# Performance work log

Hardware: AMD Instinct MI355X
Metric: run time of the kernel (lower is better)

## Reference

```python
import jax, jax.numpy as jnp
import numpy as np

NUM_HEADS = 8
LN_EPS = 1e-5


def _positional_encoding(pos_index, d_pe):
    # standard sinusoidal PE, positions start at 1; sin on even cols, cos on odd cols
    pos = pos_index.astype(jnp.float32)[:, None]                      # [N,1]
    freqs = jnp.exp(jnp.arange(0, d_pe, 2, dtype=jnp.float32) * (-np.log(10000.0) / d_pe))
    ang = pos * freqs                                                 # [N, d_pe//2]
    return jnp.stack([jnp.sin(ang), jnp.cos(ang)], axis=-1).reshape(pos.shape[0], d_pe)


def setup_inputs() -> dict:
    EMB, POS, DEV, B = 512, 64, 448, 64
    lengths = np.where(np.arange(B) % 2 == 0, 128, 256)               # ragged group sizes
    state_index = jnp.asarray(np.concatenate([[0], np.cumsum(lengths)]), dtype=jnp.int32)
    total = int(lengths.sum())                                        # 12288
    ks = jax.random.split(jax.random.key(0), 5)
    in_dim = DEV + POS
    return {
        "states": jax.random.normal(ks[0], (total, DEV), jnp.float32),
        "state_index": state_index,
        "W1": jax.random.normal(ks[1], (EMB, in_dim), jnp.float32) / np.sqrt(in_dim),
        "b1": jnp.zeros((EMB,), jnp.float32),
        "in_w": jax.random.normal(ks[2], (3 * EMB, EMB), jnp.float32) / np.sqrt(EMB),
        "in_b": jnp.zeros((3 * EMB,), jnp.float32),
        "out_w": jax.random.normal(ks[3], (EMB, EMB), jnp.float32) / np.sqrt(EMB),
        "out_b": jnp.zeros((EMB,), jnp.float32),
        "gamma": jnp.ones((EMB,), jnp.float32),
        "beta": jnp.zeros((EMB,), jnp.float32),
    }


def reference(states, state_index, W1, b1, in_w, in_b, out_w, out_b, gamma, beta):
    # --- static ragged bookkeeping from the int offsets (host-side) ---
    si = np.asarray(state_index)
    lengths = si[1:] - si[:-1]
    b = len(lengths)
    max_d = int(lengths.max())
    batch_index = jnp.asarray(np.repeat(np.arange(b), lengths), jnp.int32)   # [N]
    pos_np = np.concatenate([np.arange(1, l + 1) for l in lengths])
    pos_index = jnp.asarray(pos_np, jnp.int32)                               # [N], 1-based
    seq_idx = pos_index - 1                                                  # [N], 0-based slot

    E = W1.shape[0]
    d_pe = W1.shape[1] - states.shape[1]
    hd = E // NUM_HEADS

    # embedding MLP
    pe = _positional_encoding(pos_index, d_pe)
    x = jnp.concatenate([states, pe], axis=1)                                # [N, dev+pe]
    emb = jax.nn.leaky_relu(x @ W1.T + b1, 0.01)                             # [N, E]

    # scatter ragged tokens into padded [b, max_d, E] (zero filler, as in _reshape)
    dense = jnp.zeros((b, max_d, E), emb.dtype).at[batch_index, seq_idx].set(emb)

    # MultiheadAttention (batch_first, no padding mask -- faithful to original)
    qkv = dense @ in_w.T + in_b                                              # [b, md, 3E]
    q, k, v = jnp.split(qkv, 3, axis=-1)
    q = q.reshape(b, max_d, NUM_HEADS, hd)
    k = k.reshape(b, max_d, NUM_HEADS, hd)
    v = v.reshape(b, max_d, NUM_HEADS, hd)
    scores = jnp.einsum("bqhd,bkhd->bhqk", q, k) / np.sqrt(hd)
    attn = jax.nn.softmax(scores, axis=-1)
    ctx = jnp.einsum("bhqk,bkhd->bqhd", attn, v).reshape(b, max_d, E)
    mha_out = ctx @ out_w.T + out_b

    # residual + LayerNorm
    res = mha_out + dense
    mu = res.mean(axis=-1, keepdims=True)
    var = ((res - mu) ** 2).mean(axis=-1, keepdims=True)
    norm = (res - mu) / jnp.sqrt(var + LN_EPS) * gamma + beta

    # gather valid rows back out and concat with pre-attention embeddings
    sel = norm[batch_index, seq_idx]                                         # [N, E]
    return jnp.concatenate([emb, sel], axis=1)                               # [N, 2E]
```

## Files before the change

kernel.cpp:

```cpp
#include <hip/hip_runtime.h>

typedef unsigned short u16;
typedef __attribute__((ext_vector_type(8))) short bf16x8;
typedef __attribute__((ext_vector_type(4))) float f32x4;

__device__ __forceinline__ float bf2f(u16 u) {
    union { unsigned int i; float f; } v; v.i = ((unsigned int)u) << 16; return v.f;
}
__device__ __forceinline__ u16 f2bf(float f) {
    union { float f; unsigned int i; } v; v.f = f;
    unsigned int x = v.i;
    return (u16)((x + 0x7FFFu + ((x >> 16) & 1u)) >> 16);
}
__device__ __forceinline__ unsigned int f2bf_pk(float a, float b) {
    unsigned int r;
    asm("v_cvt_pk_bf16_f32 %0, %1, %2" : "=v"(r) : "v"(a), "v"(b));
    return r;
}

__device__ __forceinline__ bool probe_f32(const void* gamma) {
    return *(const unsigned int*)gamma == 0x3F800000u;
}
__device__ __forceinline__ float load1(const void* p, int i, bool f32) {
    return f32 ? ((const float*)p)[i] : bf2f(((const u16*)p)[i]);
}
__device__ __forceinline__ uint4 load8(const void* p, size_t e, bool f32) {
    if (f32) {
        const float* q = (const float*)p + e;
        float4 a = *(const float4*)q;
        float4 b = *(const float4*)(q + 4);
        uint4 r; u16* rp = (u16*)&r;
        rp[0] = f2bf(a.x); rp[1] = f2bf(a.y); rp[2] = f2bf(a.z); rp[3] = f2bf(a.w);
        rp[4] = f2bf(b.x); rp[5] = f2bf(b.y); rp[6] = f2bf(b.z); rp[7] = f2bf(b.w);
        return r;
    }
    return *(const uint4*)((const u16*)p + e);
}

__device__ __forceinline__ void glds16(const u16* g, u16* l) {
    __builtin_amdgcn_global_load_lds(
        (const __attribute__((address_space(1))) void*)g,
        (__attribute__((address_space(3))) void*)l, 16, 0, 0);
}

#define NTOK   12288
#define BATCH  64
#define MAXD   256
#define EMB    512
#define DEV    448

__global__ __launch_bounds__(64) void prep_xin(
        const void* __restrict__ states, const int* __restrict__ si,
        const void* __restrict__ W1, const void* __restrict__ in_w,
        const void* __restrict__ out_w, const void* __restrict__ b1,
        const void* __restrict__ in_b, const void* __restrict__ out_b,
        const void* __restrict__ gamma, const void* __restrict__ beta,
        u16* __restrict__ W1b, u16* __restrict__ in_wb, u16* __restrict__ out_wb,
        float* __restrict__ b1f, float* __restrict__ in_bf, float* __restrict__ out_bf,
        float* __restrict__ gf, float* __restrict__ bfv, u16* __restrict__ xin)
{
    bool f32 = probe_f32(gamma);
    int t = threadIdx.x;
    if (blockIdx.x < 2567) {
        int r = blockIdx.x;
        if (r < 512) {
            *(uint4*)&W1b[(size_t)r * 512 + t * 8] = load8(W1, (size_t)r * 512 + t * 8, f32);
        } else if (r < 2048) {
            int rc = r - 512;
            int h = rc / 192, rr = rc - h * 192;
            int part = rr >> 6, d = rc & 63;
            int orig = part * 512 + h * 64 + d;
            *(uint4*)&in_wb[(size_t)rc * 512 + t * 8] = load8(in_w, (size_t)orig * 512 + t * 8, f32);
        } else if (r < 2560) {
            int rc = r - 2048;
            *(uint4*)&out_wb[(size_t)rc * 512 + t * 8] = load8(out_w, (size_t)rc * 512 + t * 8, f32);
        } else if (r == 2560) {
            #pragma unroll
            for (int u = 0; u < 8; ++u) b1f[t * 8 + u] = load1(b1, t * 8 + u, f32);
        } else if (r < 2564) {
            int base = (r - 2561) * 512 + t * 8;
            #pragma unroll
            for (int u = 0; u < 8; ++u) {
                int j = base + u;
                int h = j / 192, rr = j - h * 192;
                int part = rr >> 6, d = j & 63;
                int orig = part * 512 + h * 64 + d;
                in_bf[j] = load1(in_b, orig, f32);
            }
        } else if (r == 2564) {
            #pragma unroll
            for (int u = 0; u < 8; ++u) out_bf[t * 8 + u] = load1(out_b, t * 8 + u, f32);
        } else if (r == 2565) {
            #pragma unroll
            for (int u = 0; u < 8; ++u) gf[t * 8 + u] = load1(gamma, t * 8 + u, f32);
        } else {
            #pragma unroll
            for (int u = 0; u < 8; ++u) bfv[t * 8 + u] = load1(beta, t * 8 + u, f32);
        }
    } else {
        int n = blockIdx.x - 2567;
        __shared__ int ssi[65];
        ssi[t] = si[t];
        if (t == 0) ssi[64] = si[64];
        __syncthreads();
        int lo = 0, hi = 64;
        while (hi - lo > 1) { int mid = (lo + hi) >> 1; if (ssi[mid] <= n) lo = mid; else hi = mid; }
        float pos = (float)(n - ssi[lo] + 1);
        if (t < 56) {
            *(uint4*)&xin[(size_t)n * 512 + t * 8] = load8(states, (size_t)n * DEV + t * 8, f32);
        } else {
            int j0 = (t - 56) * 8;
            uint4 vu; u16* vp = (u16*)&vu;
            #pragma unroll
            for (int jj = 0; jj < 8; ++jj) {
                int j = j0 + jj;
                int i = j >> 1;
                float freq = __expf(-0.2878231366f * (float)i);
                float ang = pos * freq;
                vp[jj] = f2bf((j & 1) ? cosf(ang) : sinf(ang));
            }
            *(uint4*)&xin[(size_t)n * 512 + DEV + j0] = vu;
        }
    }
}

template<int MODE>
__global__ __launch_bounds__(256) void gemm_glds(
        const u16* __restrict__ A, const u16* __restrict__ B,
        const float* __restrict__ bias, u16* __restrict__ C)
{
    constexpr int LDC = (MODE == 1) ? 1536 : 512;
    __shared__ __align__(16) u16 Ash[128 * 32];
    __shared__ __align__(16) u16 Bsh[128 * 32];
    __shared__ __align__(16) u16 Csh[4 * 32 * 72];

    int tid = threadIdx.x;
    int bm0 = blockIdx.y * 128, bn0 = blockIdx.x * 128;
    int lane = tid & 63, w = tid >> 6;
    int wm = (w >> 1) * 64, wn = (w & 1) * 64;
    int q = lane >> 4, m16 = lane & 15;
    int lr = lane >> 2, lc = (lane & 3) * 8;

    f32x4 acc[4][4];
    #pragma unroll
    for (int i = 0; i < 4; ++i)
        #pragma unroll
        for (int j = 0; j < 4; ++j) acc[i][j] = (f32x4){0.f, 0.f, 0.f, 0.f};

    const u16* Ab = A + (size_t)(bm0 + w * 16 + lr) * 512 + lc;
    const u16* Bb = B + (size_t)(bn0 + w * 16 + lr) * 512 + lc;
    u16* AshW = &Ash[(w * 16) * 32];
    u16* BshW = &Bsh[(w * 16) * 32];

    for (int k0 = 0; k0 < 512; k0 += 32) {
        __syncthreads();
        glds16(Ab + k0, AshW);
        glds16(Ab + (size_t)64 * 512 + k0, AshW + 64 * 32);
        glds16(Bb + k0, BshW);
        glds16(Bb + (size_t)64 * 512 + k0, BshW + 64 * 32);
        __syncthreads();
        bf16x8 af[4], bfr[4];
        #pragma unroll
        for (int i = 0; i < 4; ++i)
            af[i] = *(const bf16x8*)&Ash[(wm + i * 16 + m16) * 32 + q * 8];
        #pragma unroll
        for (int j = 0; j < 4; ++j)
            bfr[j] = *(const bf16x8*)&Bsh[(wn + j * 16 + m16) * 32 + q * 8];
        #pragma unroll
        for (int i = 0; i < 4; ++i)
            #pragma unroll
            for (int j = 0; j < 4; ++j)
                acc[i][j] = __builtin_amdgcn_mfma_f32_16x16x32_bf16(af[i], bfr[j], acc[i][j], 0, 0, 0);
    }

    u16* cw = &Csh[w * 32 * 72];
    float bv[4];
    #pragma unroll
    for (int j = 0; j < 4; ++j) bv[j] = bias[bn0 + wn + j * 16 + m16];

    int rrl = lane >> 3;
    int rcc = (lane & 7) * 8;

    #pragma unroll
    for (int ch = 0; ch < 2; ++ch) {
        #pragma unroll
        for (int ii = 0; ii < 2; ++ii) {
            int i = ch * 2 + ii;
            #pragma unroll
            for (int j = 0; j < 4; ++j) {
                float v0 = acc[i][j][0] + bv[j];
                float v1 = acc[i][j][1] + bv[j];
                float v2 = acc[i][j][2] + bv[j];
                float v3 = acc[i][j][3] + bv[j];
                if constexpr (MODE == 0) {
                    v0 = v0 >= 0.f ? v0 : 0.01f * v0;
                    v1 = v1 >= 0.f ? v1 : 0.01f * v1;
                    v2 = v2 >= 0.f ? v2 : 0.01f * v2;
                    v3 = v3 >= 0.f ? v3 : 0.01f * v3;
                }
                unsigned int pk01 = f2bf_pk(v0, v1);
                unsigned int pk23 = f2bf_pk(v2, v3);
                int rb = ii * 16 + q * 4;
                int cl = j * 16 + m16;
                cw[(rb + 0) * 72 + cl] = (u16)pk01;
                cw[(rb + 1) * 72 + cl] = (u16)(pk01 >> 16);
                cw[(rb + 2) * 72 + cl] = (u16)pk23;
                cw[(rb + 3) * 72 + cl] = (u16)(pk23 >> 16);
            }
        }
        #pragma unroll
        for (int p = 0; p < 4; ++p) {
            int row_l = p * 8 + rrl;
            uint4 v = *(const uint4*)&cw[row_l * 72 + rcc];
            int grow = bm0 + wm + ch * 32 + row_l;
            *(uint4*)&C[(size_t)grow * LDC + bn0 + wn + rcc] = v;
        }
    }
}

template<int LEN>
__global__ __launch_bounds__(512) void attn_mfma(
        const u16* __restrict__ qkv, const int* __restrict__ si,
        const float* __restrict__ in_bf, u16* __restrict__ ctx)
{
    constexpr int NT   = LEN / 16;
    constexpr int KS   = LEN / 32;
    constexpr int NPAD = 256 - LEN;
    constexpr int KSTR = 72;
    constexpr int VTS  = LEN + 8;

    __shared__ __align__(16) u16 Ksh[LEN * KSTR];
    __shared__ __align__(16) u16 Vt[64 * VTS];
    __shared__ __align__(16) u16 PshBuf[8 * 16 * VTS];
    __shared__ float kbsh[64];
    __shared__ float apsh[8][16];

    int h = blockIdx.x;
    int b = blockIdx.y * 2 + (LEN == 256 ? 1 : 0);
    int tid = threadIdx.x;
    int tok0 = si[b];
    int bb = h * 192;

    if (NPAD > 0 && tid < 64) kbsh[tid] = in_bf[bb + 64 + tid];

    constexpr int nIter = LEN * 8 / 512;
    #pragma unroll
    for (int it = 0; it < nIter; ++it) {
        int idx = tid + it * 512;
        int row = idx >> 3, c8 = (idx & 7) * 8;
        const u16* src = qkv + (size_t)(tok0 + row) * 1536 + bb;
        uint4 kv = *(const uint4*)(src + 64 + c8);
        *(uint4*)&Ksh[row * KSTR + c8] = kv;
        uint4 vv = *(const uint4*)(src + 128 + c8);
        const unsigned int* vw = (const unsigned int*)&vv;
        #pragma unroll
        for (int u = 0; u < 4; ++u)
            *(unsigned int*)&PshBuf[row * 66 + c8 + 2 * u] = vw[u];
    }
    __syncthreads();
    constexpr int SHIFT = (LEN == 256) ? 7 : 6;
    constexpr int tIter = (64 * (LEN / 2)) / 512;
    #pragma unroll
    for (int it = 0; it < tIter; ++it) {
        int idx = tid + it * 512;
        int d = idx >> SHIFT, kp = idx & (LEN / 2 - 1);
        unsigned int lo = PshBuf[(2 * kp) * 66 + d];
        unsigned int hi = PshBuf[(2 * kp + 1) * 66 + d];
        *(unsigned int*)&Vt[d * VTS + 2 * kp] = (hi << 16) | lo;
    }
    __syncthreads();

    int lane = tid & 63, w = tid >> 6;
    int m16 = lane & 15, quad = lane >> 4;
    int wq = w >> 2, wr = w & 3;
    int qt = (LEN == 256) ? blockIdx.z * 2 + wq : wq;
    u16* Psh = &PshBuf[w * 16 * VTS];

    int qrow = qt * 64 + wr * 16 + m16;
    const u16* qptr = qkv + (size_t)(tok0 + qrow) * 1536 + bb;
    bf16x8 aq0 = *(const bf16x8*)(qptr + quad * 8);
    bf16x8 aq1 = *(const bf16x8*)(qptr + 32 + quad * 8);

    if (NPAD > 0) {
        float apv = 0.f;
        #pragma unroll
        for (int j = 0; j < 8; ++j) {
            apv += bf2f((u16)aq0[j]) * kbsh[quad * 8 + j];
            apv += bf2f((u16)aq1[j]) * kbsh[32 + quad * 8 + j];
        }
        apv += __shfl_xor(apv, 16);
        apv += __shfl_xor(apv, 32);
        if (lane < 16) apsh[w][lane] = apv * 0.125f;
    }

    f32x4 sfr[NT];
    #pragma unroll
    for (int nt = 0; nt < NT; ++nt) sfr[nt] = (f32x4){0.f, 0.f, 0.f, 0.f};
    #pragma unroll
    for (int nt = 0; nt < NT; ++nt) {
        const u16* kr = &Ksh[(nt * 16 + m16) * KSTR + quad * 8];
        bf16x8 bk0 = *(const bf16x8*)(kr);
        bf16x8 bk1 = *(const bf16x8*)(kr + 32);
        sfr[nt] = __builtin_amdgcn_mfma_f32_16x16x32_bf16(aq0, bk0, sfr[nt], 0, 0, 0);
        sfr[nt] = __builtin_amdgcn_mfma_f32_16x16x32_bf16(aq1, bk1, sfr[nt], 0, 0, 0);
    }

    float pwv[4];
    #pragma unroll
    for (int reg = 0; reg < 4; ++reg) {
        float mx = -3.0e38f;
        #pragma unroll
        for (int nt = 0; nt < NT; ++nt) mx = fmaxf(mx, sfr[nt][reg]);
        mx *= 0.125f;
        float ap = 0.f;
        if (NPAD > 0) { ap = apsh[w][quad * 4 + reg]; mx = fmaxf(mx, ap); }
        #pragma unroll
        for (int off = 8; off >= 1; off >>= 1) mx = fmaxf(mx, __shfl_xor(mx, off));
        float p[NT];
        float sum = 0.f;
        #pragma unroll
        for (int nt = 0; nt < NT; ++nt) {
            p[nt] = __expf(sfr[nt][reg] * 0.125f - mx);
            sum += p[nt];
        }
        #pragma unroll
        for (int off = 8; off >= 1; off >>= 1) sum += __shfl_xor(sum, off);
        float padw = (NPAD > 0) ? (float)NPAD * __expf(ap - mx) : 0.f;
        float inv = __frcp_rn(sum + padw);
        pwv[reg] = padw * inv;
        #pragma unroll
        for (int nt = 0; nt < NT; ++nt)
            Psh[(quad * 4 + reg) * VTS + nt * 16 + m16] = f2bf(p[nt] * inv);
    }

    f32x4 ob[4];
    #pragma unroll
    for (int nt = 0; nt < 4; ++nt) ob[nt] = (f32x4){0.f, 0.f, 0.f, 0.f};
    #pragma unroll
    for (int ks = 0; ks < KS; ++ks) {
        bf16x8 af = *(const bf16x8*)&Psh[m16 * VTS + ks * 32 + quad * 8];
        #pragma unroll
        for (int nt = 0; nt < 4; ++nt) {
            bf16x8 bv = *(const bf16x8*)&Vt[(nt * 16 + m16) * VTS + ks * 32 + quad * 8];
            ob[nt] = __builtin_amdgcn_mfma_f32_16x16x32_bf16(af, bv, ob[nt], 0, 0, 0);
        }
    }

    int orow = tok0 + qt * 64 + wr * 16;
    #pragma unroll
    for (int nt = 0; nt < 4; ++nt) {
        int d = nt * 16 + m16;
        float vbv = (NPAD > 0) ? in_bf[bb + 128 + d] : 0.f;
        #pragma unroll
        for (int reg = 0; reg < 4; ++reg) {
            float val = ob[nt][reg];
            if (NPAD > 0) val += pwv[reg] * vbv;
            ctx[(size_t)(orow + quad * 4 + reg) * 512 + h * 64 + d] = f2bf(val);
        }
    }
}

__global__ __launch_bounds__(64) void ln_out(
        const u16* __restrict__ mha, const u16* __restrict__ emb,
        const float* __restrict__ gf, const float* __restrict__ bfv,
        void* __restrict__ out, const void* __restrict__ gamma)
{
    int n = blockIdx.x, lane = threadIdx.x;
    bool f32 = probe_f32(gamma);
    size_t base = (size_t)n * EMB + lane * 8;
    uint4 ev = *(const uint4*)&emb[base];
    uint4 mv = *(const uint4*)&mha[base];
    const u16* ep = (const u16*)&ev;
    const u16* mp = (const u16*)&mv;
    float e[8], r[8];
    float sum = 0.f, sq = 0.f;
    #pragma unroll
    for (int u = 0; u < 8; ++u) {
        e[u] = bf2f(ep[u]);
        r[u] = bf2f(mp[u]) + e[u];
        sum += r[u];
        sq += r[u] * r[u];
    }
    #pragma unroll
    for (int off = 32; off >= 1; off >>= 1) {
        sum += __shfl_xor(sum, off);
        sq  += __shfl_xor(sq, off);
    }
    float mu = sum * (1.f / 512.f);
    float var = sq * (1.f / 512.f) - mu * mu;
    float rstd = rsqrtf(var + 1e-5f);

    float4 g0 = *(const float4*)(gf + lane * 8);
    float4 g1 = *(const float4*)(gf + lane * 8 + 4);
    float4 be0 = *(const float4*)(bfv + lane * 8);
    float4 be1 = *(const float4*)(bfv + lane * 8 + 4);
    float g[8] = {g0.x, g0.y, g0.z, g0.w, g1.x, g1.y, g1.z, g1.w};
    float bb[8] = {be0.x, be0.y, be0.z, be0.w, be1.x, be1.y, be1.z, be1.w};
    float o[8];
    #pragma unroll
    for (int u = 0; u < 8; ++u) o[u] = (r[u] - mu) * rstd * g[u] + bb[u];

    if (f32) {
        float* op = (float*)out + (size_t)n * 1024 + lane * 8;
        *(float4*)(op)           = make_float4(e[0], e[1], e[2], e[3]);
        *(float4*)(op + 4)       = make_float4(e[4], e[5], e[6], e[7]);
        *(float4*)(op + 512)     = make_float4(o[0], o[1], o[2], o[3]);
        *(float4*)(op + 516)     = make_float4(o[4], o[5], o[6], o[7]);
    } else {
        u16* op = (u16*)out + (size_t)n * 1024 + lane * 8;
        uint4 v1, v2;
        unsigned int* w1 = (unsigned int*)&v1;
        unsigned int* w2 = (unsigned int*)&v2;
        #pragma unroll
        for (int u = 0; u < 4; ++u) {
            w1[u] = f2bf_pk(e[2 * u], e[2 * u + 1]);
            w2[u] = f2bf_pk(o[2 * u], o[2 * u + 1]);
        }
        *(uint4*)(op)       = v1;
        *(uint4*)(op + 512) = v2;
    }
}

extern "C" void kernel_launch(void* const* d_in, const int* in_sizes, int n_in,
                              void* d_out, int out_size, void* d_ws, size_t ws_size,
                              hipStream_t stream) {
    const void* states = d_in[0];
    const int*  si     = (const int*)d_in[1];
    const void* W1     = d_in[2];
    const void* b1     = d_in[3];
    const void* in_w   = d_in[4];
    const void* in_b   = d_in[5];
    const void* out_w  = d_in[6];
    const void* out_b  = d_in[7];
    const void* gamma  = d_in[8];
    const void* beta   = d_in[9];

    char* ws = (char*)d_ws;
    u16* emb    = (u16*)(ws);
    u16* xin    = (u16*)(ws + 12582912);
    u16* mha    = xin;
    u16* qkvF   = (u16*)(ws + 25165824);
    u16* W1b    = (u16*)(ws + 62914560);
    u16* in_wb  = (u16*)(ws + 63438848);
    u16* out_wb = (u16*)(ws + 65011712);
    float* b1f    = (float*)(ws + 65536000);
    float* in_bf  = (float*)(ws + 65538048);
    float* out_bf = (float*)(ws + 65544192);
    float* gf     = (float*)(ws + 65546240);
    float* bfv    = (float*)(ws + 65548288);

    u16* ctx = (u16*)d_out;

    prep_xin<<<2567 + NTOK, 64, 0, stream>>>(states, si, W1, in_w, out_w, b1, in_b, out_b,
                                             gamma, beta, W1b, in_wb, out_wb,
                                             b1f, in_bf, out_bf, gf, bfv, xin);
    gemm_glds<0><<<dim3(4, 96), 256, 0, stream>>>(xin, W1b, b1f, emb);
    gemm_glds<1><<<dim3(12, 96), 256, 0, stream>>>(emb, in_wb, in_bf, qkvF);
    attn_mfma<128><<<dim3(8, 32, 1), 512, 0, stream>>>(qkvF, si, in_bf, ctx);
    attn_mfma<256><<<dim3(8, 32, 2), 512, 0, stream>>>(qkvF, si, in_bf, ctx);
    gemm_glds<2><<<dim3(4, 96), 256, 0, stream>>>(ctx, out_wb, out_bf, mha);
    ln_out<<<NTOK, 64, 0, stream>>>(mha, emb, gf, bfv, d_out, gamma);
}
```

Baseline: 201.0 us.

## Fuse out-projection GEMM with residual LayerNorm and merge attention launches

Replaces the separate out-projection GEMM and LayerNorm kernels with one kernel. Each block computes full 512-wide rows for 32 tokens, then does the residual add, the row statistics reduction through LDS, and writes both output halves. This removes the mha intermediate round trip and one launch. The two attention template launches are merged into one grid, and prep_xin now packs four rows per 256-thread block to cut block count. The fused GEMM uses only 384 blocks with a single-buffered K loop, so it risks lower occupancy and less latency hiding than the original tiled GEMM.

```diff
diff --git a/kernel.cpp b/kernel.cpp
--- a/kernel.cpp
+++ b/kernel.cpp
@@ -49,7 +49,7 @@
 #define EMB    512
 #define DEV    448
 
-__global__ __launch_bounds__(64) void prep_xin(
+__global__ __launch_bounds__(256) void prep_xin(
         const void* __restrict__ states, const int* __restrict__ si,
         const void* __restrict__ W1, const void* __restrict__ in_w,
         const void* __restrict__ out_w, const void* __restrict__ b1,
@@ -60,9 +60,11 @@
         float* __restrict__ gf, float* __restrict__ bfv, u16* __restrict__ xin)
 {
     bool f32 = probe_f32(gamma);
-    int t = threadIdx.x;
-    if (blockIdx.x < 2567) {
-        int r = blockIdx.x;
+    int tid = threadIdx.x;
+    int t = tid & 63, w = tid >> 6;
+    if (blockIdx.x < 642) {
+        int r = blockIdx.x * 4 + w;
+        if (r >= 2567) return;
         if (r < 512) {
             *(uint4*)&W1b[(size_t)r * 512 + t * 8] = load8(W1, (size_t)r * 512 + t * 8, f32);
         } else if (r < 2048) {
@@ -98,11 +100,10 @@
             for (int u = 0; u < 8; ++u) bfv[t * 8 + u] = load1(beta, t * 8 + u, f32);
         }
     } else {
-        int n = blockIdx.x - 2567;
         __shared__ int ssi[65];
-        ssi[t] = si[t];
-        if (t == 0) ssi[64] = si[64];
+        if (tid < 65) ssi[tid] = si[tid];
         __syncthreads();
+        int n = (blockIdx.x - 642) * 4 + w;
         int lo = 0, hi = 64;
         while (hi - lo > 1) { int mid = (lo + hi) >> 1; if (ssi[mid] <= n) lo = mid; else hi = mid; }
         float pos = (float)(n - ssi[lo] + 1);
@@ -219,9 +220,11 @@
 }
 
 template<int LEN>
-__global__ __launch_bounds__(512) void attn_mfma(
+__device__ __forceinline__ void attn_body(
         const u16* __restrict__ qkv, const int* __restrict__ si,
-        const float* __restrict__ in_bf, u16* __restrict__ ctx)
+        const float* __restrict__ in_bf, u16* __restrict__ ctx,
+        u16* Ksh, u16* Vt, u16* PshBuf, float* kbsh, float (*apsh)[16],
+        int h, int b, int z)
 {
     constexpr int NT   = LEN / 16;
     constexpr int KS   = LEN / 32;
@@ -229,14 +232,6 @@
     constexpr int KSTR = 72;
     constexpr int VTS  = LEN + 8;
 
-    __shared__ __align__(16) u16 Ksh[LEN * KSTR];
-    __shared__ __align__(16) u16 Vt[64 * VTS];
-    __shared__ __align__(16) u16 PshBuf[8 * 16 * VTS];
-    __shared__ float kbsh[64];
-    __shared__ float apsh[8][16];
-
-    int h = blockIdx.x;
-    int b = blockIdx.y * 2 + (LEN == 256 ? 1 : 0);
     int tid = threadIdx.x;
     int tok0 = si[b];
     int bb = h * 192;
@@ -273,7 +268,7 @@
     int lane = tid & 63, w = tid >> 6;
     int m16 = lane & 15, quad = lane >> 4;
     int wq = w >> 2, wr = w & 3;
-    int qt = (LEN == 256) ? blockIdx.z * 2 + wq : wq;
+    int qt = (LEN == 256) ? z * 2 + wq : wq;
     u16* Psh = &PshBuf[w * 16 * VTS];
 
     int qrow = qt * 64 + wr * 16 + m16;
@@ -360,64 +355,167 @@
     }
 }
 
-__global__ __launch_bounds__(64) void ln_out(
-        const u16* __restrict__ mha, const u16* __restrict__ emb,
+__global__ __launch_bounds__(512) void attn_all(
+        const u16* __restrict__ qkv, const int* __restrict__ si,
+        const float* __restrict__ in_bf, u16* __restrict__ ctx)
+{
+    __shared__ __align__(16) u16 Ksh[256 * 72];
+    __shared__ __align__(16) u16 Vt[64 * 264];
+    __shared__ __align__(16) u16 PshBuf[8 * 16 * 264];
+    __shared__ float kbsh[64];
+    __shared__ float apsh[8][16];
+    int h = blockIdx.x;
+    if (blockIdx.y < 32) {
+        attn_body<128>(qkv, si, in_bf, ctx, Ksh, Vt, PshBuf, kbsh, apsh, h, blockIdx.y * 2, 0);
+    } else {
+        int idx = blockIdx.y - 32;
+        attn_body<256>(qkv, si, in_bf, ctx, Ksh, Vt, PshBuf, kbsh, apsh, h, (idx >> 1) * 2 + 1, idx & 1);
+    }
+}
+
+__global__ __launch_bounds__(256) void gemm_ln(
+        const u16* __restrict__ A, const u16* __restrict__ B,
+        const float* __restrict__ bias, const u16* __restrict__ emb,
         const float* __restrict__ gf, const float* __restrict__ bfv,
         void* __restrict__ out, const void* __restrict__ gamma)
 {
-    int n = blockIdx.x, lane = threadIdx.x;
+    __shared__ __align__(16) u16 sh[17408];
+    __shared__ float rsum[4][32];
+    __shared__ float rsq[4][32];
+
     bool f32 = probe_f32(gamma);
-    size_t base = (size_t)n * EMB + lane * 8;
-    uint4 ev = *(const uint4*)&emb[base];
-    uint4 mv = *(const uint4*)&mha[base];
-    const u16* ep = (const u16*)&ev;
-    const u16* mp = (const u16*)&mv;
-    float e[8], r[8];
-    float sum = 0.f, sq = 0.f;
-    #pragma unroll
-    for (int u = 0; u < 8; ++u) {
-        e[u] = bf2f(ep[u]);
-        r[u] = bf2f(mp[u]) + e[u];
-        sum += r[u];
-        sq += r[u] * r[u];
-    }
-    #pragma unroll
-    for (int off = 32; off >= 1; off >>= 1) {
-        sum += __shfl_xor(sum, off);
-        sq  += __shfl_xor(sq, off);
-    }
-    float mu = sum * (1.f / 512.f);
-    float var = sq * (1.f / 512.f) - mu * mu;
-    float rstd = rsqrtf(var + 1e-5f);
-
-    float4 g0 = *(const float4*)(gf + lane * 8);
-    float4 g1 = *(const float4*)(gf + lane * 8 + 4);
-    float4 be0 = *(const float4*)(bfv + lane * 8);
-    float4 be1 = *(const float4*)(bfv + lane * 8 + 4);
-    float g[8] = {g0.x, g0.y, g0.z, g0.w, g1.x, g1.y, g1.z, g1.w};
-    float bb[8] = {be0.x, be0.y, be0.z, be0.w, be1.x, be1.y, be1.z, be1.w};
-    float o[8];
-    #pragma unroll
-    for (int u = 0; u < 8; ++u) o[u] = (r[u] - mu) * rstd * g[u] + bb[u];
-
-    if (f32) {
-        float* op = (float*)out + (size_t)n * 1024 + lane * 8;
-        *(float4*)(op)           = make_float4(e[0], e[1], e[2], e[3]);
-        *(float4*)(op + 4)       = make_float4(e[4], e[5], e[6], e[7]);
-        *(float4*)(op + 512)     = make_float4(o[0], o[1], o[2], o[3]);
-        *(float4*)(op + 516)     = make_float4(o[4], o[5], o[6], o[7]);
-    } else {
-        u16* op = (u16*)out + (size_t)n * 1024 + lane * 8;
-        uint4 v1, v2;
-        unsigned int* w1 = (unsigned int*)&v1;
-        unsigned int* w2 = (unsigned int*)&v2;
-        #pragma unroll
-        for (int u = 0; u < 4; ++u) {
-            w1[u] = f2bf_pk(e[2 * u], e[2 * u + 1]);
-            w2[u] = f2bf_pk(o[2 * u], o[2 * u + 1]);
-        }
-        *(uint4*)(op)       = v1;
-        *(uint4*)(op + 512) = v2;
+    int tid = threadIdx.x;
+    int lane = tid & 63, w = tid >> 6;
+    int bm0 = blockIdx.x * 32;
+    int q = lane >> 4, m16 = lane & 15;
+    int lr = lane >> 2, lc = (lane & 3) * 8;
+    int wn = w * 128;
+
+    u16* Ash = sh;
+    u16* Bsh = sh + 1024;
+    u16* Esh = sh;
+
+    f32x4 acc[2][8];
+    #pragma unroll
+    for (int i = 0; i < 2; ++i)
+        #pragma unroll
+        for (int j = 0; j < 8; ++j) acc[i][j] = (f32x4){0.f, 0.f, 0.f, 0.f};
+
+    const u16* Abase = A + (size_t)(bm0 + (w & 1) * 16 + lr) * 512 + lc;
+    const u16* Bbase = B + (size_t)(wn + lr) * 512 + lc;
+    u16* AshW = &Ash[((w & 1) * 16) * 32];
+
+    for (int k0 = 0; k0 < 512; k0 += 32) {
+        __syncthreads();
+        if (w < 2) glds16(Abase + k0, AshW);
+        #pragma unroll
+        for (int it = 0; it < 8; ++it)
+            glds16(Bbase + (size_t)(it * 16) * 512 + k0, &Bsh[(wn + it * 16) * 32]);
+        __syncthreads();
+        bf16x8 af[2], bfr[8];
+        #pragma unroll
+        for (int i = 0; i < 2; ++i)
+            af[i] = *(const bf16x8*)&Ash[(i * 16 + m16) * 32 + q * 8];
+        #pragma unroll
+        for (int j = 0; j < 8; ++j)
+            bfr[j] = *(const bf16x8*)&Bsh[(wn + j * 16 + m16) * 32 + q * 8];
+        #pragma unroll
+        for (int i = 0; i < 2; ++i)
+            #pragma unroll
+            for (int j = 0; j < 8; ++j)
+                acc[i][j] = __builtin_amdgcn_mfma_f32_16x16x32_bf16(af[i], bfr[j], acc[i][j], 0, 0, 0);
+    }
+
+    float bv[8], gv[8], bev[8];
+    #pragma unroll
+    for (int j = 0; j < 8; ++j) {
+        int c = wn + j * 16 + m16;
+        bv[j] = bias[c]; gv[j] = gf[c]; bev[j] = bfv[c];
+    }
+
+    __syncthreads();
+
+    #pragma unroll
+    for (int it = 0; it < 8; ++it) {
+        int idx = tid + it * 256;
+        int r = idx >> 6, c8 = (idx & 63) * 8;
+        uint4 ev = *(const uint4*)&emb[(size_t)(bm0 + r) * 512 + c8];
+        *(uint4*)&Esh[r * 520 + c8] = ev;
+        if (f32) {
+            const u16* ep = (const u16*)&ev;
+            float* op = (float*)out + (size_t)(bm0 + r) * 1024 + c8;
+            *(float4*)(op)     = make_float4(bf2f(ep[0]), bf2f(ep[1]), bf2f(ep[2]), bf2f(ep[3]));
+            *(float4*)(op + 4) = make_float4(bf2f(ep[4]), bf2f(ep[5]), bf2f(ep[6]), bf2f(ep[7]));
+        } else {
+            *(uint4*)((u16*)out + (size_t)(bm0 + r) * 1024 + c8) = ev;
+        }
+    }
+    __syncthreads();
+
+    #pragma unroll
+    for (int i = 0; i < 2; ++i) {
+        #pragma unroll
+        for (int reg = 0; reg < 4; ++reg) {
+            int row = i * 16 + q * 4 + reg;
+            float s = 0.f, ss = 0.f;
+            #pragma unroll
+            for (int j = 0; j < 8; ++j) {
+                float rv = acc[i][j][reg] + bv[j] + bf2f(Esh[row * 520 + wn + j * 16 + m16]);
+                s += rv; ss += rv * rv;
+            }
+            #pragma unroll
+            for (int off = 8; off >= 1; off >>= 1) {
+                s  += __shfl_xor(s, off);
+                ss += __shfl_xor(ss, off);
+            }
+            if (m16 == 0) { rsum[w][row] = s; rsq[w][row] = ss; }
+        }
+    }
+    __syncthreads();
+
+    float muv[2][4], rsv[2][4];
+    #pragma unroll
+    for (int i = 0; i < 2; ++i) {
+        #pragma unroll
+        for (int reg = 0; reg < 4; ++reg) {
+            int row = i * 16 + q * 4 + reg;
+            float t  = rsum[0][row] + rsum[1][row] + rsum[2][row] + rsum[3][row];
+            float tq = rsq[0][row]  + rsq[1][row]  + rsq[2][row]  + rsq[3][row];
+            float m = t * (1.f / 512.f);
+            muv[i][reg] = m;
+            rsv[i][reg] = rsqrtf(tq * (1.f / 512.f) - m * m + 1e-5f);
+        }
+    }
+
+    #pragma unroll
+    for (int i = 0; i < 2; ++i) {
+        #pragma unroll
+        for (int reg = 0; reg < 4; ++reg) {
+            int row = i * 16 + q * 4 + reg;
+            #pragma unroll
+            for (int j = 0; j < 8; ++j) {
+                int idx = row * 520 + wn + j * 16 + m16;
+                float rv = acc[i][j][reg] + bv[j] + bf2f(Esh[idx]);
+                float nv = (rv - muv[i][reg]) * rsv[i][reg] * gv[j] + bev[j];
+                Esh[idx] = f2bf(nv);
+            }
+        }
+    }
+    __syncthreads();
+
+    #pragma unroll
+    for (int it = 0; it < 8; ++it) {
+        int idx = tid + it * 256;
+        int r = idx >> 6, c8 = (idx & 63) * 8;
+        uint4 v = *(const uint4*)&Esh[r * 520 + c8];
+        if (f32) {
+            const u16* vp = (const u16*)&v;
+            float* op = (float*)out + (size_t)(bm0 + r) * 1024 + 512 + c8;
+            *(float4*)(op)     = make_float4(bf2f(vp[0]), bf2f(vp[1]), bf2f(vp[2]), bf2f(vp[3]));
+            *(float4*)(op + 4) = make_float4(bf2f(vp[4]), bf2f(vp[5]), bf2f(vp[6]), bf2f(vp[7]));
+        } else {
+            *(uint4*)((u16*)out + (size_t)(bm0 + r) * 1024 + 512 + c8) = v;
+        }
     }
 }
 
@@ -438,7 +536,6 @@
     char* ws = (char*)d_ws;
     u16* emb    = (u16*)(ws);
     u16* xin    = (u16*)(ws + 12582912);
-    u16* mha    = xin;
     u16* qkvF   = (u16*)(ws + 25165824);
     u16* W1b    = (u16*)(ws + 62914560);
     u16* in_wb  = (u16*)(ws + 63438848);
@@ -448,16 +545,13 @@
     float* out_bf = (float*)(ws + 65544192);
     float* gf     = (float*)(ws + 65546240);
     float* bfv    = (float*)(ws + 65548288);
-
-    u16* ctx = (u16*)d_out;
-
-    prep_xin<<<2567 + NTOK, 64, 0, stream>>>(states, si, W1, in_w, out_w, b1, in_b, out_b,
-                                             gamma, beta, W1b, in_wb, out_wb,
-                                             b1f, in_bf, out_bf, gf, bfv, xin);
+    u16* ctx    = (u16*)(ws + 67108864);
+
+    prep_xin<<<3714, 256, 0, stream>>>(states, si, W1, in_w, out_w, b1, in_b, out_b,
+                                       gamma, beta, W1b, in_wb, out_wb,
+                                       b1f, in_bf, out_bf, gf, bfv, xin);
     gemm_glds<0><<<dim3(4, 96), 256, 0, stream>>>(xin, W1b, b1f, emb);
     gemm_glds<1><<<dim3(12, 96), 256, 0, stream>>>(emb, in_wb, in_bf, qkvF);
-    attn_mfma<128><<<dim3(8, 32, 1), 512, 0, stream>>>(qkvF, si, in_bf, ctx);
-    attn_mfma<256><<<dim3(8, 32, 2), 512, 0, stream>>>(qkvF, si, in_bf, ctx);
-    gemm_glds<2><<<dim3(4, 96), 256, 0, stream>>>(ctx, out_wb, out_bf, mha);
-    ln_out<<<NTOK, 64, 0, stream>>>(mha, emb, gf, bfv, d_out, gamma);
-}
+    attn_all<<<dim3(8, 96), 512, 0, stream>>>(qkvF, si, in_bf, ctx);
+    gemm_ln<<<384, 256, 0, stream>>>(ctx, out_wb, out_bf, emb, gf, bfv, d_out, gamma);
+}
```

New measurement: 220.2 us. +9.6%, slower.

## Merge attention launches and pack four rows per block in prep and LN

Applied to the files above, without the earlier changes.

The two attention kernels (length 128 and 256) become one launch that branches on blockIdx.y, with shared memory sized for the larger case. The prep and layernorm kernels now run four 64-lane rows per 256-thread block instead of one row per 64-thread block, which cuts the block count fourfold. The context buffer moves from the output buffer to workspace. The merged attention kernel always allocates the larger shared-memory footprint, which may lower occupancy for the length-128 blocks.

```diff
diff --git a/kernel.cpp b/kernel.cpp
--- a/kernel.cpp
+++ b/kernel.cpp
@@ -49,7 +49,7 @@
 #define EMB    512
 #define DEV    448
 
-__global__ __launch_bounds__(64) void prep_xin(
+__global__ __launch_bounds__(256) void prep_xin(
         const void* __restrict__ states, const int* __restrict__ si,
         const void* __restrict__ W1, const void* __restrict__ in_w,
         const void* __restrict__ out_w, const void* __restrict__ b1,
@@ -60,9 +60,11 @@
         float* __restrict__ gf, float* __restrict__ bfv, u16* __restrict__ xin)
 {
     bool f32 = probe_f32(gamma);
-    int t = threadIdx.x;
-    if (blockIdx.x < 2567) {
-        int r = blockIdx.x;
+    int tid = threadIdx.x;
+    int t = tid & 63, w = tid >> 6;
+    if (blockIdx.x < 642) {
+        int r = blockIdx.x * 4 + w;
+        if (r >= 2567) return;
         if (r < 512) {
             *(uint4*)&W1b[(size_t)r * 512 + t * 8] = load8(W1, (size_t)r * 512 + t * 8, f32);
         } else if (r < 2048) {
@@ -98,11 +100,10 @@
             for (int u = 0; u < 8; ++u) bfv[t * 8 + u] = load1(beta, t * 8 + u, f32);
         }
     } else {
-        int n = blockIdx.x - 2567;
         __shared__ int ssi[65];
-        ssi[t] = si[t];
-        if (t == 0) ssi[64] = si[64];
+        if (tid < 65) ssi[tid] = si[tid];
         __syncthreads();
+        int n = (blockIdx.x - 642) * 4 + w;
         int lo = 0, hi = 64;
         while (hi - lo > 1) { int mid = (lo + hi) >> 1; if (ssi[mid] <= n) lo = mid; else hi = mid; }
         float pos = (float)(n - ssi[lo] + 1);
@@ -219,9 +220,11 @@
 }
 
 template<int LEN>
-__global__ __launch_bounds__(512) void attn_mfma(
+__device__ __forceinline__ void attn_body(
         const u16* __restrict__ qkv, const int* __restrict__ si,
-        const float* __restrict__ in_bf, u16* __restrict__ ctx)
+        const float* __restrict__ in_bf, u16* __restrict__ ctx,
+        u16* Ksh, u16* Vt, u16* PshBuf, float* kbsh, float (*apsh)[16],
+        int h, int b, int z)
 {
     constexpr int NT   = LEN / 16;
     constexpr int KS   = LEN / 32;
@@ -229,14 +232,6 @@
     constexpr int KSTR = 72;
     constexpr int VTS  = LEN + 8;
 
-    __shared__ __align__(16) u16 Ksh[LEN * KSTR];
-    __shared__ __align__(16) u16 Vt[64 * VTS];
-    __shared__ __align__(16) u16 PshBuf[8 * 16 * VTS];
-    __shared__ float kbsh[64];
-    __shared__ float apsh[8][16];
-
-    int h = blockIdx.x;
-    int b = blockIdx.y * 2 + (LEN == 256 ? 1 : 0);
     int tid = threadIdx.x;
     int tok0 = si[b];
     int bb = h * 192;
@@ -273,7 +268,7 @@
     int lane = tid & 63, w = tid >> 6;
     int m16 = lane & 15, quad = lane >> 4;
     int wq = w >> 2, wr = w & 3;
-    int qt = (LEN == 256) ? blockIdx.z * 2 + wq : wq;
+    int qt = (LEN == 256) ? z * 2 + wq : wq;
     u16* Psh = &PshBuf[w * 16 * VTS];
 
     int qrow = qt * 64 + wr * 16 + m16;
@@ -360,12 +355,32 @@
     }
 }
 
-__global__ __launch_bounds__(64) void ln_out(
+__global__ __launch_bounds__(512) void attn_all(
+        const u16* __restrict__ qkv, const int* __restrict__ si,
+        const float* __restrict__ in_bf, u16* __restrict__ ctx)
+{
+    __shared__ __align__(16) u16 Ksh[256 * 72];
+    __shared__ __align__(16) u16 Vt[64 * 264];
+    __shared__ __align__(16) u16 PshBuf[8 * 16 * 264];
+    __shared__ float kbsh[64];
+    __shared__ float apsh[8][16];
+    int h = blockIdx.x;
+    if (blockIdx.y < 32) {
+        attn_body<128>(qkv, si, in_bf, ctx, Ksh, Vt, PshBuf, kbsh, apsh, h, blockIdx.y * 2, 0);
+    } else {
+        int idx = blockIdx.y - 32;
+        attn_body<256>(qkv, si, in_bf, ctx, Ksh, Vt, PshBuf, kbsh, apsh, h, (idx >> 1) * 2 + 1, idx & 1);
+    }
+}
+
+__global__ __launch_bounds__(256) void ln_out(
         const u16* __restrict__ mha, const u16* __restrict__ emb,
         const float* __restrict__ gf, const float* __restrict__ bfv,
         void* __restrict__ out, const void* __restrict__ gamma)
 {
-    int n = blockIdx.x, lane = threadIdx.x;
+    int tid = threadIdx.x;
+    int lane = tid & 63, w = tid >> 6;
+    int n = blockIdx.x * 4 + w;
     bool f32 = probe_f32(gamma);
     size_t base = (size_t)n * EMB + lane * 8;
     uint4 ev = *(const uint4*)&emb[base];
@@ -448,16 +463,14 @@
     float* out_bf = (float*)(ws + 65544192);
     float* gf     = (float*)(ws + 65546240);
     float* bfv    = (float*)(ws + 65548288);
-
-    u16* ctx = (u16*)d_out;
-
-    prep_xin<<<2567 + NTOK, 64, 0, stream>>>(states, si, W1, in_w, out_w, b1, in_b, out_b,
-                                             gamma, beta, W1b, in_wb, out_wb,
-                                             b1f, in_bf, out_bf, gf, bfv, xin);
+    u16* ctx    = (u16*)(ws + 67108864);
+
+    prep_xin<<<3714, 256, 0, stream>>>(states, si, W1, in_w, out_w, b1, in_b, out_b,
+                                       gamma, beta, W1b, in_wb, out_wb,
+                                       b1f, in_bf, out_bf, gf, bfv, xin);
     gemm_glds<0><<<dim3(4, 96), 256, 0, stream>>>(xin, W1b, b1f, emb);
     gemm_glds<1><<<dim3(12, 96), 256, 0, stream>>>(emb, in_wb, in_bf, qkvF);
-    attn_mfma<128><<<dim3(8, 32, 1), 512, 0, stream>>>(qkvF, si, in_bf, ctx);
-    attn_mfma<256><<<dim3(8, 32, 2), 512, 0, stream>>>(qkvF, si, in_bf, ctx);
+    attn_all<<<dim3(8, 96), 512, 0, stream>>>(qkvF, si, in_bf, ctx);
     gemm_glds<2><<<dim3(4, 96), 256, 0, stream>>>(ctx, out_wb, out_bf, mha);
-    ln_out<<<NTOK, 64, 0, stream>>>(mha, emb, gf, bfv, d_out, gamma);
-}
+    ln_out<<<3072, 256, 0, stream>>>(mha, emb, gf, bfv, d_out, gamma);
+}
```

Measured after the change: 197.4 us. About the same (-1.8%).
